# Performance work log

Measured on AMD Instinct MI355X. Metric: run time of the kernel, lower is better.

Reference implementation:

```python
import jax, jax.numpy as jnp
import numpy as np

B, S, H, E, K = 4, 2048, 1024, 8, 2

def setup_inputs() -> dict:
    key = jax.random.key(0)
    k0, k1, k2, k3 = jax.random.split(key, 4)
    x = jax.random.normal(k0, (B, S, H), dtype=jnp.float32)
    # xavier-uniform-like scales
    router_w = jax.random.normal(k1, (E, H), dtype=jnp.float32) * np.float32(1.0 / np.sqrt(H))
    xav1 = np.float32(np.sqrt(2.0 / (2 * H + H)))
    w1 = jax.random.normal(k2, (E, 2 * H, H), dtype=jnp.float32) * xav1
    w2 = jax.random.normal(k3, (E, H, 2 * H), dtype=jnp.float32) * xav1
    return {"x": x, "router_w": router_w, "w1": w1, "w2": w2}

def reference(x, router_w, w1, w2):
    bsz, seq, hidden = x.shape
    n_experts = w1.shape[0]
    tokens = x.reshape(-1, hidden)                      # [T, H]
    T = tokens.shape[0]
    logits = tokens @ router_w.T                        # [T, E]
    topv, topi = jax.lax.top_k(logits, K)               # [T, K]
    w = jax.nn.softmax(topv, axis=-1).astype(tokens.dtype)
    # Dense gate matrix: gate[t, e] = routing weight of expert e for token t
    # (zero for non-selected experts). Equivalent to the torch pad/dispatch/
    # scatter-add combine: padded slots have weight 0 and contribute nothing.
    gate = jnp.zeros((T, n_experts), tokens.dtype).at[jnp.arange(T)[:, None], topi].add(w)
    out = jnp.zeros_like(tokens)
    for e in range(n_experts):  # small fixed expert count
        h = jax.nn.gelu(tokens @ w1[e].T, approximate=False)  # [T, 2H] (torch F.gelu = erf)
        y = h @ w2[e].T                                       # [T, H]
        out = out + gate[:, e:e + 1] * y
    return out.reshape(bsz, seq, hidden)
```

## Files before the change

### kernel.cpp

```cpp
#include <hip/hip_runtime.h>
#include <stdint.h>
#include <math.h>

#define T_TOK 8192
#define H_DIM 1024
#define H2    2048
#define NE    8

typedef unsigned short u16;
typedef __attribute__((ext_vector_type(8))) short bf16x8;
typedef __attribute__((ext_vector_type(4))) float f32x4;

__device__ __forceinline__ u16 f32_to_bf16(float f) {
  union { float f; unsigned u; } c; c.f = f;
  unsigned u = c.u + 0x7fffu + ((c.u >> 16) & 1u);
  return (u16)(u >> 16);
}
__device__ __forceinline__ float bf2f(u16 v) {
  union { unsigned u; float f; } c; c.u = (unsigned)v << 16; return c.f;
}

__device__ __forceinline__ float fast_gelu(float v) {
  float u = v * v;
  float z2 = v * fmaf(u, 0.1029437f, 2.3022078f);
  float e = __builtin_amdgcn_exp2f(z2);
  float r = __builtin_amdgcn_rcpf(1.0f + e);
  return v - v * r;
}

__device__ __forceinline__ void g2l16(const void* g, void* l) {
  __builtin_amdgcn_global_load_lds(
      (const __attribute__((address_space(1))) unsigned*)g,
      (__attribute__((address_space(3))) unsigned*)l, 16, 0, 0);
}

__device__ __forceinline__ int prefix_base(const int* counts, int e) {
  int b = 0;
#pragma unroll
  for (int j = 0; j < NE; j++) b += (j < e) ? counts[j] : 0;
  return b;
}

__global__ __launch_bounds__(256) void prep_kernel(
    const float* __restrict__ x, const float* __restrict__ rw,
    const float* __restrict__ w1,
    u16* __restrict__ xb, u16* __restrict__ w1b,
    int* __restrict__ tope, float2* __restrict__ gate2,
    int* __restrict__ counts) {
  int blk = blockIdx.x;
  if (blk == 0 && threadIdx.x < NE) counts[threadIdx.x] = 0;

  {
    const float4* s4 = (const float4*)w1;
    int b0 = blk * 2048 + threadIdx.x;
#pragma unroll
    for (int k = 0; k < 8; ++k) {
      int i = b0 + k * 256;
      float4 v = s4[i];
      *(ushort4*)(w1b + (size_t)i * 4) = make_ushort4(
          f32_to_bf16(v.x), f32_to_bf16(v.y), f32_to_bf16(v.z), f32_to_bf16(v.w));
    }
  }

  int wave = threadIdx.x >> 6;
  int lane = threadIdx.x & 63;
  int t = blk * 4 + wave;
  const float4* x4 = (const float4*)(x + (size_t)t * H_DIM);
  const float4* rw4 = (const float4*)rw;
  u16* xbrow = xb + (size_t)t * H_DIM;

  double acc[NE];
#pragma unroll
  for (int e = 0; e < NE; e++) acc[e] = 0.0;
#pragma unroll
  for (int i = 0; i < 4; i++) {
    int c = lane + 64 * i;
    float4 xv = x4[c];
    ushort4 bv = make_ushort4(f32_to_bf16(xv.x), f32_to_bf16(xv.y),
                              f32_to_bf16(xv.z), f32_to_bf16(xv.w));
    *(ushort4*)(xbrow + c * 4) = bv;
#pragma unroll
    for (int e = 0; e < NE; e++) {
      float4 wv = rw4[e * 256 + c];
      acc[e] += (double)xv.x * wv.x + (double)xv.y * wv.y +
                (double)xv.z * wv.z + (double)xv.w * wv.w;
    }
  }
#pragma unroll
  for (int off = 32; off >= 1; off >>= 1)
#pragma unroll
    for (int e = 0; e < NE; e++) acc[e] += __shfl_xor(acc[e], off, 64);

  if (lane == 0) {
    int e0 = 0; double v0 = acc[0];
#pragma unroll
    for (int e = 1; e < NE; e++) if (acc[e] > v0) { v0 = acc[e]; e0 = e; }
    int e1 = -1; double v1 = -1e300;
#pragma unroll
    for (int e = 0; e < NE; e++) if (e != e0 && acc[e] > v1) { v1 = acc[e]; e1 = e; }
    double ex = exp(v1 - v0);
    tope[t] = e0 | (e1 << 8);
    gate2[t] = make_float2((float)(1.0 / (1.0 + ex)), (float)(ex / (1.0 + ex)));
  }
}

__global__ __launch_bounds__(256) void build_kernel(
    const int* __restrict__ tope, int* __restrict__ counts,
    int* __restrict__ tok_list, int2* __restrict__ pos2) {
  __shared__ int cts[4][NE];
  __shared__ int gbase[NE];
  int tid = threadIdx.x, lane = tid & 63, w = tid >> 6;
  int t = blockIdx.x * 256 + tid;
  int pk = tope[t];
  int e0 = pk & 0xff, e1 = (pk >> 8) & 0xff;
  unsigned long long lt = ((unsigned long long)1 << lane) - 1;

  int r0 = 0, r1 = 0;
#pragma unroll
  for (int e = 0; e < NE; e++) {
    unsigned long long b0 = __ballot(e0 == e);
    unsigned long long b1 = __ballot(e1 == e);
    int n0 = __popcll(b0), n1 = __popcll(b1);
    if (e0 == e) r0 = __popcll(b0 & lt);
    if (e1 == e) r1 = n0 + __popcll(b1 & lt);
    if (lane == 0) cts[w][e] = n0 + n1;
  }
  __syncthreads();
  if (tid < NE) {
    int bt = cts[0][tid] + cts[1][tid] + cts[2][tid] + cts[3][tid];
    gbase[tid] = atomicAdd(&counts[tid], bt);
  }
  __syncthreads();
  int off0 = gbase[e0] + r0;
  int off1 = gbase[e1] + r1;
#pragma unroll
  for (int wp = 0; wp < 4; wp++) {
    if (wp < w) { off0 += cts[wp][e0]; off1 += cts[wp][e1]; }
  }
  tok_list[e0 * T_TOK + off0] = t;
  tok_list[e1 * T_TOK + off1] = t;
  pos2[t] = make_int2(off0, off1);
}

template <int NKT, int NT, int OUTN, bool GATHER, bool GELU, bool CVTW2>
__global__ __launch_bounds__(512, 1) void moe_gemm(
    const u16* __restrict__ A, const u16* __restrict__ W,
    u16* __restrict__ O, const int* __restrict__ tok_list,
    const int* __restrict__ counts,
    const float* __restrict__ cvt_src, u16* __restrict__ cvt_dst) {
  if (CVTW2) {
    const float4* s4 = (const float4*)cvt_src;
    int b0 = blockIdx.x * 2048 + threadIdx.x;
#pragma unroll
    for (int k = 0; k < 4; ++k) {
      int i = b0 + k * 512;
      float4 v = s4[i];
      *(ushort4*)(cvt_dst + (size_t)i * 4) = make_ushort4(
          f32_to_bf16(v.x), f32_to_bf16(v.y), f32_to_bf16(v.z), f32_to_bf16(v.w));
    }
  }
  int e = blockIdx.x & 7;
  int rem = blockIdx.x >> 3;
  int mt = rem / NT, nt = rem % NT;
  int cnt = counts[e];
  int m0 = mt * 256;
  if (m0 >= cnt) return;
  int base = prefix_base(counts, e);
  const int K = NKT * 64;

  __shared__ u16 lA[2][16384];
  __shared__ u16 lB[2][16384];

  int tid = threadIdx.x;
  int ln = tid & 63, w = tid >> 6;
  int wr = w >> 2, wc = w & 3;
  int quad = ln >> 4, l16 = ln & 15;

  const u16* We = W + (size_t)e * OUTN * K;
  const u16* aptr[4]; const u16* bptr[4];
#pragma unroll
  for (int c = 0; c < 4; ++c) {
    int u = c * 512 + tid;
    int row = u >> 3;
    int chunk = (u & 7) ^ (row & 7);
    int ar = m0 + row; if (ar > cnt - 1) ar = cnt - 1;
    const u16* ab;
    if (GATHER) ab = A + (size_t)tok_list[e * T_TOK + ar] * K;
    else        ab = A + (size_t)(base + ar) * K;
    aptr[c] = ab + chunk * 8;
    bptr[c] = We + (size_t)(nt * 256 + row) * K + chunk * 8;
  }

  int adA[8][2], adB[4][2];
#pragma unroll
  for (int f = 0; f < 8; ++f) {
    int r = wr * 128 + f * 16 + l16;
#pragma unroll
    for (int kk = 0; kk < 2; ++kk)
      adA[f][kk] = r * 64 + ((((kk << 2) | quad) ^ (r & 7)) << 3);
  }
#pragma unroll
  for (int j = 0; j < 4; ++j) {
    int r = wc * 64 + j * 16 + l16;
#pragma unroll
    for (int kk = 0; kk < 2; ++kk)
      adB[j][kk] = r * 64 + ((((kk << 2) | quad) ^ (r & 7)) << 3);
  }

  f32x4 acc[8][4];
#pragma unroll
  for (int i = 0; i < 8; i++)
#pragma unroll
    for (int j = 0; j < 4; j++)
#pragma unroll
      for (int r = 0; r < 4; r++) acc[i][j][r] = 0.f;

#pragma unroll
  for (int c = 0; c < 4; ++c) {
    g2l16(aptr[c], &lA[0][(c * 512 + tid) * 8]);
    g2l16(bptr[c], &lB[0][(c * 512 + tid) * 8]);
  }

#pragma unroll 1
  for (int t = 0; t < NKT; ++t) {
    int d = t & 1;
    asm volatile("s_waitcnt vmcnt(0)" ::: "memory");
    __builtin_amdgcn_s_barrier();
    __builtin_amdgcn_sched_barrier(0);

    const u16* Ab = &lA[d][0];
    const u16* Bb = &lB[d][0];
    bf16x8 af[8], af2[8], bf[4], bf2v[4];
    af[0]  = *(const bf16x8*)(Ab + adA[0][0]);
    af2[0] = *(const bf16x8*)(Ab + adA[0][1]);
#pragma unroll
    for (int j = 0; j < 4; ++j) {
      bf[j]   = *(const bf16x8*)(Bb + adB[j][0]);
      bf2v[j] = *(const bf16x8*)(Bb + adB[j][1]);
    }
#pragma unroll
    for (int f = 1; f < 8; ++f) {
      af[f]  = *(const bf16x8*)(Ab + adA[f][0]);
      af2[f] = *(const bf16x8*)(Ab + adA[f][1]);
    }

    if (t + 1 < NKT) {
#pragma unroll
      for (int c = 0; c < 4; ++c) {
        g2l16(aptr[c] + (t + 1) * 64, &lA[d ^ 1][(c * 512 + tid) * 8]);
        g2l16(bptr[c] + (t + 1) * 64, &lB[d ^ 1][(c * 512 + tid) * 8]);
      }
    }
    __builtin_amdgcn_sched_barrier(0);

    __builtin_amdgcn_s_setprio(1);
#pragma unroll
    for (int mi = 0; mi < 8; ++mi) {
#pragma unroll
      for (int ni = 0; ni < 4; ++ni)
        acc[mi][ni] = __builtin_amdgcn_mfma_f32_16x16x32_bf16(
            af[mi], bf[ni], acc[mi][ni], 0, 0, 0);
#pragma unroll
      for (int ni = 0; ni < 4; ++ni)
        acc[mi][ni] = __builtin_amdgcn_mfma_f32_16x16x32_bf16(
            af2[mi], bf2v[ni], acc[mi][ni], 0, 0, 0);
    }
    __builtin_amdgcn_s_setprio(0);
  }

#pragma unroll
  for (int mi = 0; mi < 8; ++mi) {
    int rb = wr * 128 + mi * 16 + quad * 4;
#pragma unroll
    for (int r = 0; r < 4; ++r) {
      int grow = m0 + rb + r;
      if (grow < cnt) {
        size_t o = (size_t)(base + grow) * OUTN + nt * 256 + wc * 64 + l16;
#pragma unroll
        for (int ni = 0; ni < 4; ++ni) {
          float v = acc[mi][ni][r];
          if (GELU) v = fast_gelu(v);
          O[o + ni * 16] = f32_to_bf16(v);
        }
      }
    }
  }
}

__global__ __launch_bounds__(256) void combine_kernel(
    const u16* __restrict__ y, const int* __restrict__ tope,
    const float2* __restrict__ gate2, const int2* __restrict__ pos2,
    const int* __restrict__ counts, float* __restrict__ out) {
  int t = blockIdx.x;
  int pk = tope[t];
  int e0 = pk & 0xff, e1 = (pk >> 8) & 0xff;
  float2 g = gate2[t];
  int2 p = pos2[t];
  int hb0 = prefix_base(counts, e0);
  int hb1 = prefix_base(counts, e1);
  size_t s0 = (size_t)(hb0 + p.x) * H_DIM + threadIdx.x * 4;
  size_t s1 = (size_t)(hb1 + p.y) * H_DIM + threadIdx.x * 4;
  ushort4 a = *(const ushort4*)(y + s0);
  ushort4 b = *(const ushort4*)(y + s1);
  float4 o;
  o.x = g.x * bf2f(a.x) + g.y * bf2f(b.x);
  o.y = g.x * bf2f(a.y) + g.y * bf2f(b.y);
  o.z = g.x * bf2f(a.z) + g.y * bf2f(b.z);
  o.w = g.x * bf2f(a.w) + g.y * bf2f(b.w);
  *(float4*)(out + (size_t)t * H_DIM + threadIdx.x * 4) = o;
}

extern "C" void kernel_launch(void* const* d_in, const int* in_sizes, int n_in,
                              void* d_out, int out_size, void* d_ws, size_t ws_size,
                              hipStream_t stream) {
  const float* x  = (const float*)d_in[0];
  const float* rw = (const float*)d_in[1];
  const float* w1 = (const float*)d_in[2];
  const float* w2 = (const float*)d_in[3];
  float* out = (float*)d_out;

  char* ws = (char*)d_ws;
  u16* xb       = (u16*)(ws);
  u16* w1b      = (u16*)(ws + 16777216);
  u16* y        = (u16*)(ws + 16777216);
  u16* w2b      = (u16*)(ws + 50331648);
  u16* h        = (u16*)(ws + 83886080);
  int* tok_list = (int*)(ws + 150994944);
  int* tope     = (int*)(ws + 151257088);
  float2* gate2 = (float2*)(ws + 151289856);
  int2* pos2    = (int2*)(ws + 151355392);
  int* counts   = (int*)(ws + 151420928);

  prep_kernel<<<T_TOK / 4, 256, 0, stream>>>(x, rw, w1, xb, w1b,
                                             tope, gate2, counts);
  build_kernel<<<T_TOK / 256, 256, 0, stream>>>(tope, counts, tok_list, pos2);
  moe_gemm<16, 8, H2, true, true, true>
      <<<NE * 32 * 8, 512, 0, stream>>>(xb, w1b, h, tok_list, counts, w2, w2b);
  moe_gemm<32, 4, H_DIM, false, false, false>
      <<<NE * 32 * 4, 512, 0, stream>>>(h, w2b, y, tok_list, counts,
                                        nullptr, nullptr);
  combine_kernel<<<T_TOK, 256, 0, stream>>>(y, tope, gate2, pos2, counts, out);
}
```

Measured before the change: 378.0 us.

## Fuse gated combine into second GEMM epilogue via atomics, rebalance weight conversion

The combine kernel and the bf16 intermediate y buffer are removed. The second expert GEMM now multiplies each result by its routing gate and atomically adds it in fp32 into the output, which prep_kernel zeroes first. The w1 conversion moves from prep_kernel into extra blocks of build_kernel. The w2 conversion is moved onto the idle upper-M-tile blocks of the first GEMM, which would otherwise exit early because of their token count. This saves a kernel launch and the y write/read round trip, but adds global float atomics, whose summation order is nondeterministic, plus the cost of zeroing the output.

```diff
diff --git a/kernel.cpp b/kernel.cpp
--- a/kernel.cpp
+++ b/kernel.cpp
@@ -43,23 +43,17 @@
 
 __global__ __launch_bounds__(256) void prep_kernel(
     const float* __restrict__ x, const float* __restrict__ rw,
-    const float* __restrict__ w1,
-    u16* __restrict__ xb, u16* __restrict__ w1b,
-    int* __restrict__ tope, float2* __restrict__ gate2,
-    int* __restrict__ counts) {
+    u16* __restrict__ xb, int* __restrict__ tope, float2* __restrict__ gate2,
+    int* __restrict__ counts, float* __restrict__ out_zero) {
   int blk = blockIdx.x;
   if (blk == 0 && threadIdx.x < NE) counts[threadIdx.x] = 0;
 
   {
-    const float4* s4 = (const float4*)w1;
-    int b0 = blk * 2048 + threadIdx.x;
-#pragma unroll
-    for (int k = 0; k < 8; ++k) {
-      int i = b0 + k * 256;
-      float4 v = s4[i];
-      *(ushort4*)(w1b + (size_t)i * 4) = make_ushort4(
-          f32_to_bf16(v.x), f32_to_bf16(v.y), f32_to_bf16(v.z), f32_to_bf16(v.w));
-    }
+    float4 z = make_float4(0.f, 0.f, 0.f, 0.f);
+    float4* o4 = (float4*)out_zero;
+    int b0 = blk * 1024 + threadIdx.x;
+#pragma unroll
+    for (int k = 0; k < 4; ++k) o4[b0 + k * 256] = z;
   }
 
   int wave = threadIdx.x >> 6;
@@ -106,7 +100,20 @@
 
 __global__ __launch_bounds__(256) void build_kernel(
     const int* __restrict__ tope, int* __restrict__ counts,
-    int* __restrict__ tok_list, int2* __restrict__ pos2) {
+    int* __restrict__ tok_list,
+    const float* __restrict__ w1, u16* __restrict__ w1b) {
+  if (blockIdx.x >= 32) {
+    const float4* s4 = (const float4*)w1;
+    int b0 = (blockIdx.x - 32) * 2048 + threadIdx.x;
+#pragma unroll
+    for (int k = 0; k < 8; ++k) {
+      int i = b0 + k * 256;
+      float4 v = s4[i];
+      *(ushort4*)(w1b + (size_t)i * 4) = make_ushort4(
+          f32_to_bf16(v.x), f32_to_bf16(v.y), f32_to_bf16(v.z), f32_to_bf16(v.w));
+    }
+    return;
+  }
   __shared__ int cts[4][NE];
   __shared__ int gbase[NE];
   int tid = threadIdx.x, lane = tid & 63, w = tid >> 6;
@@ -139,29 +146,32 @@
   }
   tok_list[e0 * T_TOK + off0] = t;
   tok_list[e1 * T_TOK + off1] = t;
-  pos2[t] = make_int2(off0, off1);
-}
-
-template <int NKT, int NT, int OUTN, bool GATHER, bool GELU, bool CVTW2>
+}
+
+template <int NKT, int NT, int OUTN, bool GATHER, bool GELU, bool CVTW2,
+          bool FUSEOUT>
 __global__ __launch_bounds__(512, 1) void moe_gemm(
     const u16* __restrict__ A, const u16* __restrict__ W,
     u16* __restrict__ O, const int* __restrict__ tok_list,
     const int* __restrict__ counts,
-    const float* __restrict__ cvt_src, u16* __restrict__ cvt_dst) {
-  if (CVTW2) {
+    const float* __restrict__ cvt_src, u16* __restrict__ cvt_dst,
+    const int* __restrict__ tope, const float2* __restrict__ gate2,
+    float* __restrict__ fout) {
+  int e = blockIdx.x & 7;
+  int rem = blockIdx.x >> 3;
+  int mt = rem / NT, nt = rem % NT;
+  if (CVTW2 && mt >= 16) {
+    int cid = e * (16 * NT) + (mt - 16) * NT + nt;
     const float4* s4 = (const float4*)cvt_src;
-    int b0 = blockIdx.x * 2048 + threadIdx.x;
-#pragma unroll
-    for (int k = 0; k < 4; ++k) {
+    int b0 = cid * 4096 + threadIdx.x;
+#pragma unroll
+    for (int k = 0; k < 8; ++k) {
       int i = b0 + k * 512;
       float4 v = s4[i];
       *(ushort4*)(cvt_dst + (size_t)i * 4) = make_ushort4(
           f32_to_bf16(v.x), f32_to_bf16(v.y), f32_to_bf16(v.z), f32_to_bf16(v.w));
     }
   }
-  int e = blockIdx.x & 7;
-  int rem = blockIdx.x >> 3;
-  int mt = rem / NT, nt = rem % NT;
   int cnt = counts[e];
   int m0 = mt * 256;
   if (m0 >= cnt) return;
@@ -275,39 +285,27 @@
     for (int r = 0; r < 4; ++r) {
       int grow = m0 + rb + r;
       if (grow < cnt) {
-        size_t o = (size_t)(base + grow) * OUTN + nt * 256 + wc * 64 + l16;
-#pragma unroll
-        for (int ni = 0; ni < 4; ++ni) {
-          float v = acc[mi][ni][r];
-          if (GELU) v = fast_gelu(v);
-          O[o + ni * 16] = f32_to_bf16(v);
+        if (FUSEOUT) {
+          int tk = tope ? tok_list[e * T_TOK + grow] : 0;
+          int pk = tope[tk];
+          float2 gg = gate2[tk];
+          float g = ((pk & 0xff) == e) ? gg.x : gg.y;
+          float* orow = fout + (size_t)tk * H_DIM + nt * 256 + wc * 64 + l16;
+#pragma unroll
+          for (int ni = 0; ni < 4; ++ni)
+            atomicAdd(orow + ni * 16, g * acc[mi][ni][r]);
+        } else {
+          size_t o = (size_t)(base + grow) * OUTN + nt * 256 + wc * 64 + l16;
+#pragma unroll
+          for (int ni = 0; ni < 4; ++ni) {
+            float v = acc[mi][ni][r];
+            if (GELU) v = fast_gelu(v);
+            O[o + ni * 16] = f32_to_bf16(v);
+          }
         }
       }
     }
   }
-}
-
-__global__ __launch_bounds__(256) void combine_kernel(
-    const u16* __restrict__ y, const int* __restrict__ tope,
-    const float2* __restrict__ gate2, const int2* __restrict__ pos2,
-    const int* __restrict__ counts, float* __restrict__ out) {
-  int t = blockIdx.x;
-  int pk = tope[t];
-  int e0 = pk & 0xff, e1 = (pk >> 8) & 0xff;
-  float2 g = gate2[t];
-  int2 p = pos2[t];
-  int hb0 = prefix_base(counts, e0);
-  int hb1 = prefix_base(counts, e1);
-  size_t s0 = (size_t)(hb0 + p.x) * H_DIM + threadIdx.x * 4;
-  size_t s1 = (size_t)(hb1 + p.y) * H_DIM + threadIdx.x * 4;
-  ushort4 a = *(const ushort4*)(y + s0);
-  ushort4 b = *(const ushort4*)(y + s1);
-  float4 o;
-  o.x = g.x * bf2f(a.x) + g.y * bf2f(b.x);
-  o.y = g.x * bf2f(a.y) + g.y * bf2f(b.y);
-  o.z = g.x * bf2f(a.z) + g.y * bf2f(b.z);
-  o.w = g.x * bf2f(a.w) + g.y * bf2f(b.w);
-  *(float4*)(out + (size_t)t * H_DIM + threadIdx.x * 4) = o;
 }
 
 extern "C" void kernel_launch(void* const* d_in, const int* in_sizes, int n_in,
@@ -322,22 +320,20 @@
   char* ws = (char*)d_ws;
   u16* xb       = (u16*)(ws);
   u16* w1b      = (u16*)(ws + 16777216);
-  u16* y        = (u16*)(ws + 16777216);
   u16* w2b      = (u16*)(ws + 50331648);
   u16* h        = (u16*)(ws + 83886080);
   int* tok_list = (int*)(ws + 150994944);
   int* tope     = (int*)(ws + 151257088);
   float2* gate2 = (float2*)(ws + 151289856);
-  int2* pos2    = (int2*)(ws + 151355392);
-  int* counts   = (int*)(ws + 151420928);
-
-  prep_kernel<<<T_TOK / 4, 256, 0, stream>>>(x, rw, w1, xb, w1b,
-                                             tope, gate2, counts);
-  build_kernel<<<T_TOK / 256, 256, 0, stream>>>(tope, counts, tok_list, pos2);
-  moe_gemm<16, 8, H2, true, true, true>
-      <<<NE * 32 * 8, 512, 0, stream>>>(xb, w1b, h, tok_list, counts, w2, w2b);
-  moe_gemm<32, 4, H_DIM, false, false, false>
-      <<<NE * 32 * 4, 512, 0, stream>>>(h, w2b, y, tok_list, counts,
-                                        nullptr, nullptr);
-  combine_kernel<<<T_TOK, 256, 0, stream>>>(y, tope, gate2, pos2, counts, out);
-}
+  int* counts   = (int*)(ws + 151355392);
+
+  prep_kernel<<<T_TOK / 4, 256, 0, stream>>>(x, rw, xb, tope, gate2, counts,
+                                             out);
+  build_kernel<<<32 + 2048, 256, 0, stream>>>(tope, counts, tok_list, w1, w1b);
+  moe_gemm<16, 8, H2, true, true, true, false>
+      <<<NE * 32 * 8, 512, 0, stream>>>(xb, w1b, h, tok_list, counts, w2, w2b,
+                                        nullptr, nullptr, nullptr);
+  moe_gemm<32, 4, H_DIM, false, false, false, true>
+      <<<NE * 32 * 4, 512, 0, stream>>>(h, w2b, nullptr, tok_list, counts,
+                                        nullptr, nullptr, tope, gate2, out);
+}
```

New measurement: 421.2 us. 1.11x slower.
